# Optimization experiments

Hardware: AMD Instinct MI355X
Metric: run time of the kernel (lower is better)

## Reference

```python
import jax, jax.numpy as jnp
import numpy as np

H = 256   # encoder/decoder hidden size
U = 128   # attention units


def setup_inputs() -> dict:
    key = jax.random.key(0)
    ks = jax.random.split(key, 8)
    B, Td, Te = 16, 128, 1024
    s = 1.0 / np.sqrt(H)
    return {
        "dec_outputs": jax.random.normal(ks[0], (B, Td, H), dtype=jnp.float32),
        "enc_outputs": jax.random.normal(ks[1], (B, Te, H), dtype=jnp.float32),
        "W1": jax.random.normal(ks[2], (H, U), dtype=jnp.float32) * s,
        "b1": jnp.zeros((U,), dtype=jnp.float32),
        "W2": jax.random.normal(ks[3], (H, U), dtype=jnp.float32) * s,
        "b2": jnp.zeros((U,), dtype=jnp.float32),
        "V": jax.random.normal(ks[4], (U, 1), dtype=jnp.float32) * (1.0 / np.sqrt(U)),
        "bv": jnp.zeros((1,), dtype=jnp.float32),
    }


def reference(dec_outputs, enc_outputs, W1, b1, W2, b2, V, bv):
    # Project once (the original redundantly re-projects enc_outputs per step).
    # w1d: [B, Td, U], w2e: [B, Te, U]
    w1d = jnp.einsum("bth,hu->btu", dec_outputs, W1) + b1
    w2e = jnp.einsum("bsh,hu->bsu", enc_outputs, W2) + b2
    # Additive Bahdanau score: tanh over broadcast sum -> [B, Td, Te, U]
    feat = jnp.tanh(w1d[:, :, None, :] + w2e[:, None, :, :])
    # V projection to scalar score: [B, Td, Te]
    score = jnp.einsum("btsu,u->bts", feat, V[:, 0]) + bv[0]
    # Softmax over encoder positions (original Softmax(axis=1) on [B, Te])
    return jax.nn.softmax(score, axis=-1)
```

## Files before the change

kernel.cpp:

```cpp
#include <hip/hip_runtime.h>
#include <math.h>

#define HB 256
#define UB 128
#define BB 16
#define TD 128
#define TE 1024

#define CLAMP_W 7.0f
#define L2E2 2.8853900817779268f
#define ALPHA 1.52587890625e-05f
#define NEG2ALPHA (-3.0517578125e-05f)

#define PINV(x) asm volatile("" : "+v"(x))
#define PINS(x) asm volatile("" : "+s"(x))
#define PINV4(q) do { PINV((q).x); PINV((q).y); PINV((q).z); PINV((q).w); } while (0)
#define PINS4(q) do { PINS((q).x); PINS((q).y); PINS((q).z); PINS((q).w); } while (0)

__device__ __forceinline__ float stage_exp(float w, float shift) {
    float t = fminf(fmaxf(w, -CLAMP_W), CLAMP_W);
    return exp2f(fmaf(t, L2E2, shift));
}

#define DEC_SLABS 32
#define ENC_SLABS 256
#define DEC_BLOCKS (16 * DEC_SLABS)
#define ENC_BLOCKS (16 * ENC_SLABS)

__global__ __launch_bounds__(64) void proj_v8(
    const float* __restrict__ dec, const float* __restrict__ enc,
    const float* __restrict__ W1, const float* __restrict__ b1,
    const float* __restrict__ W2, const float* __restrict__ b2,
    float* __restrict__ Ea, float* __restrict__ Eb) {
    const int blk = blockIdx.x;
    const bool is_dec = blk < DEC_BLOCKS;
    const int rel   = is_dec ? blk : blk - DEC_BLOCKS;
    const int nslab = is_dec ? DEC_SLABS : ENC_SLABS;
    const int ut    = rel / nslab;
    const int slab  = rel - ut * nslab;
    const float* __restrict__ X    = is_dec ? dec : enc;
    const float* __restrict__ W    = is_dec ? W1 : W2;
    const float* __restrict__ bias = is_dec ? b1 : b2;

    const int l = threadIdx.x;
    const long row = (long)slab * 64 + l;
    const float* xr = X + row * HB;
    const int u0 = ut * 8;

    float acc[8];
    #pragma unroll
    for (int j = 0; j < 8; ++j) acc[j] = 0.f;

    float4 xC, xN, wC[4][2], wN[4][2];
    xC = *reinterpret_cast<const float4*>(xr);
    #pragma unroll
    for (int k = 0; k < 4; ++k) {
        wC[k][0] = *reinterpret_cast<const float4*>(W + k * UB + u0);
        wC[k][1] = *reinterpret_cast<const float4*>(W + k * UB + u0 + 4);
    }

    #pragma unroll 2
    for (int h = 0; h < HB; h += 4) {
        const int hn = (h + 4 < HB) ? h + 4 : 0;
        xN = *reinterpret_cast<const float4*>(xr + hn);
        #pragma unroll
        for (int k = 0; k < 4; ++k) {
            wN[k][0] = *reinterpret_cast<const float4*>(W + (hn + k) * UB + u0);
            wN[k][1] = *reinterpret_cast<const float4*>(W + (hn + k) * UB + u0 + 4);
        }
        const float xk[4] = {xC.x, xC.y, xC.z, xC.w};
        #pragma unroll
        for (int k = 0; k < 4; ++k) {
            acc[0] = fmaf(xk[k], wC[k][0].x, acc[0]);
            acc[1] = fmaf(xk[k], wC[k][0].y, acc[1]);
            acc[2] = fmaf(xk[k], wC[k][0].z, acc[2]);
            acc[3] = fmaf(xk[k], wC[k][0].w, acc[3]);
            acc[4] = fmaf(xk[k], wC[k][1].x, acc[4]);
            acc[5] = fmaf(xk[k], wC[k][1].y, acc[5]);
            acc[6] = fmaf(xk[k], wC[k][1].z, acc[6]);
            acc[7] = fmaf(xk[k], wC[k][1].w, acc[7]);
        }
        PINV4(xN);
        #pragma unroll
        for (int k = 0; k < 4; ++k) { PINS4(wN[k][0]); PINS4(wN[k][1]); }
        xC = xN;
        #pragma unroll
        for (int k = 0; k < 4; ++k) { wC[k][0] = wN[k][0]; wC[k][1] = wN[k][1]; }
    }

    float4 bv0 = *reinterpret_cast<const float4*>(bias + u0);
    float4 bv1 = *reinterpret_cast<const float4*>(bias + u0 + 4);
    const float sh = is_dec ? -16.f : 0.f;
    float4 q0 = make_float4(stage_exp(acc[0] + bv0.x, sh), stage_exp(acc[1] + bv0.y, sh),
                            stage_exp(acc[2] + bv0.z, sh), stage_exp(acc[3] + bv0.w, sh));
    float4 q1 = make_float4(stage_exp(acc[4] + bv1.x, sh), stage_exp(acc[5] + bv1.y, sh),
                            stage_exp(acc[6] + bv1.z, sh), stage_exp(acc[7] + bv1.w, sh));

    if (is_dec) {
        const long bq = row >> 7;
        const int  t  = (int)(row & (TD - 1));
        float4* dst = reinterpret_cast<float4*>(Ea);
        dst[(bq * 32 + ut * 2 + 0) * TD + t] = q0;
        dst[(bq * 32 + ut * 2 + 1) * TD + t] = q1;
    } else {
        const long bq = row >> 10;
        const int  s  = (int)(row & (TE - 1));
        float4* dst = reinterpret_cast<float4*>(Eb);
        dst[(bq * 32 + ut * 2 + 0) * TE + s] = q0;
        dst[(bq * 32 + ut * 2 + 1) * TE + s] = q1;
    }
}

__global__ __launch_bounds__(1024) void score_v8(
    const float* __restrict__ Ea4,
    const float4* __restrict__ Eb4,
    const float* __restrict__ V,
    float* __restrict__ out) {
    const int tid = threadIdx.x;
    const int wv = tid >> 6, l = tid & 63;
    const int i = blockIdx.x;
    const int b  = 2 * (i & 7) + ((i >> 3) >> 4);
    const int t0 = ((i >> 3) & 15) * 8;

    const float*  ab = Ea4 + ((long)b * 32 * TD) * 4;
    const float4* ep = Eb4 + (long)b * 32 * TE + tid;
    const float alphav = ALPHA;

    float acc[8];
    #pragma unroll
    for (int t = 0; t < 8; ++t) acc[t] = 0.f;

    float4 aC[8], aN[8], vC, vN, eC, eN;
#define SLOAD(AB, VB, EB, U4) do {                                        \
        const float* _a = ab + ((long)(U4) * TD + t0) * 4;                \
        _Pragma("unroll")                                                 \
        for (int t = 0; t < 8; ++t)                                       \
            AB[t] = *reinterpret_cast<const float4*>(_a + t * 4);         \
        VB = *reinterpret_cast<const float4*>(V + (U4) * 4);              \
        EB = ep[(long)(U4) * TE];                                         \
    } while (0)

#define SCOMP(AB, VB, EB) do {                                            \
        _Pragma("unroll")                                                 \
        for (int t = 0; t < 8; ++t) {                                     \
            float4 A = AB[t];                                             \
            float X0 = fmaf(A.x, (EB).x, alphav);                         \
            float X1 = fmaf(A.y, (EB).y, alphav);                         \
            float X2 = fmaf(A.z, (EB).z, alphav);                         \
            float X3 = fmaf(A.w, (EB).w, alphav);                         \
            float P01 = X0 * X1, P23 = X2 * X3;                           \
            float N01 = fmaf((VB).x, X1, (VB).y * X0);                    \
            float N23 = fmaf((VB).z, X3, (VB).w * X2);                    \
            float N   = fmaf(N01, P23, N23 * P01);                        \
            acc[t] = fmaf(N, __builtin_amdgcn_rcpf(P01 * P23), acc[t]);   \
        }                                                                 \
    } while (0)

    SLOAD(aC, vC, eC, 0);
    #pragma unroll 2
    for (int u4 = 0; u4 < 32; ++u4) {
        const int p = (u4 + 1 < 32) ? u4 + 1 : 0;
        SLOAD(aN, vN, eN, p);
        SCOMP(aC, vC, eC);
        #pragma unroll
        for (int t = 0; t < 8; ++t) PINS4(aN[t]);
        PINS4(vN);
        PINV4(eN);
        #pragma unroll
        for (int t = 0; t < 8; ++t) aC[t] = aN[t];
        vC = vN; eC = eN;
    }
#undef SLOAD
#undef SCOMP

    float sc[8];
    #pragma unroll
    for (int t = 0; t < 8; ++t) sc[t] = NEG2ALPHA * acc[t];

    __shared__ float red[8][16];
    #pragma unroll
    for (int t = 0; t < 8; ++t) {
        float x = sc[t];
        #pragma unroll
        for (int off = 32; off > 0; off >>= 1) x = fmaxf(x, __shfl_xor(x, off, 64));
        if (l == 0) red[t][wv] = x;
    }
    __syncthreads();
    float m[8];
    #pragma unroll
    for (int t = 0; t < 8; ++t) {
        float x = red[t][0];
        #pragma unroll
        for (int k = 1; k < 16; ++k) x = fmaxf(x, red[t][k]);
        m[t] = x;
    }
    __syncthreads();
    #pragma unroll
    for (int t = 0; t < 8; ++t) {
        sc[t] = __expf(sc[t] - m[t]);
        float x = sc[t];
        #pragma unroll
        for (int off = 32; off > 0; off >>= 1) x += __shfl_xor(x, off, 64);
        if (l == 0) red[t][wv] = x;
    }
    __syncthreads();
    #pragma unroll
    for (int t = 0; t < 8; ++t) {
        float x = red[t][0];
        #pragma unroll
        for (int k = 1; k < 16; ++k) x += red[t][k];
        out[((long)b * TD + t0 + t) * TE + tid] = sc[t] * (1.f / x);
    }
}

extern "C" void kernel_launch(void* const* d_in, const int* in_sizes, int n_in,
                              void* d_out, int out_size, void* d_ws, size_t ws_size,
                              hipStream_t stream) {
    const float* dec = (const float*)d_in[0];
    const float* enc = (const float*)d_in[1];
    const float* W1  = (const float*)d_in[2];
    const float* b1  = (const float*)d_in[3];
    const float* W2  = (const float*)d_in[4];
    const float* b2  = (const float*)d_in[5];
    const float* V   = (const float*)d_in[6];
    float* out = (float*)d_out;

    float* Ea = (float*)d_ws;
    float* Eb = Ea + (long)BB * 32 * TD * 4;

    proj_v8<<<DEC_BLOCKS + ENC_BLOCKS, 64, 0, stream>>>(dec, enc, W1, b1, W2, b2, Ea, Eb);
    score_v8<<<256, 1024, 0, stream>>>(Ea, (const float4*)Eb, V, out);
}
```

Baseline: 76.40 us.

## Restructure projection kernel with LDS-staged transposed input tile and split-K reduction

The projection kernel now uses 512-thread blocks, each handling a 64-row slab and half of the U outputs. The slab is loaded cooperatively with coalesced float4 reads and stored transposed into shared memory. Each wave computes 16 units over half of the H dimension, and the two halves are combined through an LDS reduction. Previously every tiny 64-thread block re-read its whole X rows once per 8-unit group; this change is meant to cut those redundant global reads and improve occupancy. The cost is extra synchronisation, scalar transposed LDS stores that may hit bank conflicts, and the loss of explicit register prefetching.

Result: faster. 67.62 us, median of 3 (-11.5%).

```diff
diff --git a/kernel.cpp b/kernel.cpp
--- a/kernel.cpp
+++ b/kernel.cpp
@@ -23,91 +23,103 @@
 }
 
 #define DEC_SLABS 32
-#define ENC_SLABS 256
-#define DEC_BLOCKS (16 * DEC_SLABS)
-#define ENC_BLOCKS (16 * ENC_SLABS)
-
-__global__ __launch_bounds__(64) void proj_v8(
+#define NSLABS 288
+#define PROJ_BLOCKS (NSLABS * 2)
+
+__global__ __launch_bounds__(512) void proj_v12(
     const float* __restrict__ dec, const float* __restrict__ enc,
     const float* __restrict__ W1, const float* __restrict__ b1,
     const float* __restrict__ W2, const float* __restrict__ b2,
     float* __restrict__ Ea, float* __restrict__ Eb) {
     const int blk = blockIdx.x;
-    const bool is_dec = blk < DEC_BLOCKS;
-    const int rel   = is_dec ? blk : blk - DEC_BLOCKS;
-    const int nslab = is_dec ? DEC_SLABS : ENC_SLABS;
-    const int ut    = rel / nslab;
-    const int slab  = rel - ut * nslab;
+    const int slab = blk >> 1, uhalf = blk & 1;
+    const bool is_dec = slab < DEC_SLABS;
+    const int rel = is_dec ? slab : slab - DEC_SLABS;
     const float* __restrict__ X    = is_dec ? dec : enc;
     const float* __restrict__ W    = is_dec ? W1 : W2;
     const float* __restrict__ bias = is_dec ? b1 : b2;
 
-    const int l = threadIdx.x;
-    const long row = (long)slab * 64 + l;
-    const float* xr = X + row * HB;
-    const int u0 = ut * 8;
-
-    float acc[8];
-    #pragma unroll
-    for (int j = 0; j < 8; ++j) acc[j] = 0.f;
-
-    float4 xC, xN, wC[4][2], wN[4][2];
-    xC = *reinterpret_cast<const float4*>(xr);
-    #pragma unroll
-    for (int k = 0; k < 4; ++k) {
-        wC[k][0] = *reinterpret_cast<const float4*>(W + k * UB + u0);
-        wC[k][1] = *reinterpret_cast<const float4*>(W + k * UB + u0 + 4);
-    }
-
-    #pragma unroll 2
-    for (int h = 0; h < HB; h += 4) {
-        const int hn = (h + 4 < HB) ? h + 4 : 0;
-        xN = *reinterpret_cast<const float4*>(xr + hn);
-        #pragma unroll
-        for (int k = 0; k < 4; ++k) {
-            wN[k][0] = *reinterpret_cast<const float4*>(W + (hn + k) * UB + u0);
-            wN[k][1] = *reinterpret_cast<const float4*>(W + (hn + k) * UB + u0 + 4);
+    __shared__ float xt[HB][66];
+    const int tid = threadIdx.x;
+    const long row0 = (long)rel * 64;
+
+    #pragma unroll
+    for (int it = 0; it < 8; ++it) {
+        int idx = it * 512 + tid;
+        int row = idx >> 6, hf4 = idx & 63;
+        float4 f = *reinterpret_cast<const float4*>(X + (row0 + row) * HB + hf4 * 4);
+        xt[hf4 * 4 + 0][row] = f.x;
+        xt[hf4 * 4 + 1][row] = f.y;
+        xt[hf4 * 4 + 2][row] = f.z;
+        xt[hf4 * 4 + 3][row] = f.w;
+    }
+    __syncthreads();
+
+    const int l = tid & 63;
+    const int w = __builtin_amdgcn_readfirstlane(tid >> 6);
+    const int ub3 = w & 3;
+    const int ub  = ub3 + uhalf * 4;
+    const int hh  = w >> 2;
+    const int u0  = ub * 16;
+    const int h0  = hh * 128;
+
+    float acc[16];
+    #pragma unroll
+    for (int j = 0; j < 16; ++j) acc[j] = 0.f;
+
+    for (int h = 0; h < 128; h += 4) {
+        const int hg = h0 + h;
+        float4 wf[4][4];
+        #pragma unroll
+        for (int k = 0; k < 4; ++k)
+            #pragma unroll
+            for (int q = 0; q < 4; ++q)
+                wf[k][q] = *reinterpret_cast<const float4*>(
+                    W + (hg + k) * UB + u0 + q * 4);
+        float xk[4];
+        #pragma unroll
+        for (int k = 0; k < 4; ++k) xk[k] = xt[hg + k][l];
+        #pragma unroll
+        for (int k = 0; k < 4; ++k)
+            #pragma unroll
+            for (int q = 0; q < 4; ++q) {
+                acc[q * 4 + 0] = fmaf(xk[k], wf[k][q].x, acc[q * 4 + 0]);
+                acc[q * 4 + 1] = fmaf(xk[k], wf[k][q].y, acc[q * 4 + 1]);
+                acc[q * 4 + 2] = fmaf(xk[k], wf[k][q].z, acc[q * 4 + 2]);
+                acc[q * 4 + 3] = fmaf(xk[k], wf[k][q].w, acc[q * 4 + 3]);
+            }
+    }
+
+    __syncthreads();
+    float4* red = reinterpret_cast<float4*>(&xt[0][0]);
+    if (hh == 1) {
+        #pragma unroll
+        for (int q = 0; q < 4; ++q)
+            red[((ub3 * 64 + l) << 2) + q] =
+                make_float4(acc[q * 4], acc[q * 4 + 1], acc[q * 4 + 2], acc[q * 4 + 3]);
+    }
+    __syncthreads();
+    if (hh == 0) {
+        #pragma unroll
+        for (int q = 0; q < 4; ++q) {
+            float4 r = red[((ub3 * 64 + l) << 2) + q];
+            acc[q * 4 + 0] += r.x; acc[q * 4 + 1] += r.y;
+            acc[q * 4 + 2] += r.z; acc[q * 4 + 3] += r.w;
         }
-        const float xk[4] = {xC.x, xC.y, xC.z, xC.w};
-        #pragma unroll
-        for (int k = 0; k < 4; ++k) {
-            acc[0] = fmaf(xk[k], wC[k][0].x, acc[0]);
-            acc[1] = fmaf(xk[k], wC[k][0].y, acc[1]);
-            acc[2] = fmaf(xk[k], wC[k][0].z, acc[2]);
-            acc[3] = fmaf(xk[k], wC[k][0].w, acc[3]);
-            acc[4] = fmaf(xk[k], wC[k][1].x, acc[4]);
-            acc[5] = fmaf(xk[k], wC[k][1].y, acc[5]);
-            acc[6] = fmaf(xk[k], wC[k][1].z, acc[6]);
-            acc[7] = fmaf(xk[k], wC[k][1].w, acc[7]);
+        const float sh = is_dec ? -16.f : 0.f;
+        const int POS  = is_dec ? TD : TE;
+        const long bq  = row0 / POS;
+        const int pos  = (int)(row0 % POS) + l;
+        float4* dst4 = reinterpret_cast<float4*>(is_dec ? Ea : Eb);
+        #pragma unroll
+        for (int q = 0; q < 4; ++q) {
+            float4 o = make_float4(
+                stage_exp(acc[q * 4 + 0] + bias[u0 + q * 4 + 0], sh),
+                stage_exp(acc[q * 4 + 1] + bias[u0 + q * 4 + 1], sh),
+                stage_exp(acc[q * 4 + 2] + bias[u0 + q * 4 + 2], sh),
+                stage_exp(acc[q * 4 + 3] + bias[u0 + q * 4 + 3], sh));
+            dst4[(bq * 32 + ub * 4 + q) * (long)POS + pos] = o;
         }
-        PINV4(xN);
-        #pragma unroll
-        for (int k = 0; k < 4; ++k) { PINS4(wN[k][0]); PINS4(wN[k][1]); }
-        xC = xN;
-        #pragma unroll
-        for (int k = 0; k < 4; ++k) { wC[k][0] = wN[k][0]; wC[k][1] = wN[k][1]; }
-    }
-
-    float4 bv0 = *reinterpret_cast<const float4*>(bias + u0);
-    float4 bv1 = *reinterpret_cast<const float4*>(bias + u0 + 4);
-    const float sh = is_dec ? -16.f : 0.f;
-    float4 q0 = make_float4(stage_exp(acc[0] + bv0.x, sh), stage_exp(acc[1] + bv0.y, sh),
-                            stage_exp(acc[2] + bv0.z, sh), stage_exp(acc[3] + bv0.w, sh));
-    float4 q1 = make_float4(stage_exp(acc[4] + bv1.x, sh), stage_exp(acc[5] + bv1.y, sh),
-                            stage_exp(acc[6] + bv1.z, sh), stage_exp(acc[7] + bv1.w, sh));
-
-    if (is_dec) {
-        const long bq = row >> 7;
-        const int  t  = (int)(row & (TD - 1));
-        float4* dst = reinterpret_cast<float4*>(Ea);
-        dst[(bq * 32 + ut * 2 + 0) * TD + t] = q0;
-        dst[(bq * 32 + ut * 2 + 1) * TD + t] = q1;
-    } else {
-        const long bq = row >> 10;
-        const int  s  = (int)(row & (TE - 1));
-        float4* dst = reinterpret_cast<float4*>(Eb);
-        dst[(bq * 32 + ut * 2 + 0) * TE + s] = q0;
-        dst[(bq * 32 + ut * 2 + 1) * TE + s] = q1;
     }
 }
 
@@ -228,6 +240,6 @@
     float* Ea = (float*)d_ws;
     float* Eb = Ea + (long)BB * 32 * TD * 4;
 
-    proj_v8<<<DEC_BLOCKS + ENC_BLOCKS, 64, 0, stream>>>(dec, enc, W1, b1, W2, b2, Ea, Eb);
+    proj_v12<<<PROJ_BLOCKS, 512, 0, stream>>>(dec, enc, W1, b1, W2, b2, Ea, Eb);
     score_v8<<<256, 1024, 0, stream>>>(Ea, (const float4*)Eb, V, out);
 }
```
